# Performance work log

Measured on AMD Instinct MI355X. Metric: run time of the kernel, lower is better.

## Reference

```python
import jax, jax.numpy as jnp
import numpy as np

B, T, I = 32, 512, 1024
H, HS = 8, 128  # n_heads, head_size; hidden = H*HS = 1024
LIM = 1.0 / np.sqrt(HS)


def setup_inputs() -> dict:
    key = jax.random.key(0)
    kx, kif, kzo, khh, kb = jax.random.split(key, 5)
    u = lambda k, shp: jax.random.uniform(k, shp, jnp.float32, -LIM, LIM)
    return {
        "xs": jax.random.normal(kx, (B, T, I), jnp.float32),
        "weight_if": u(kif, (H, 2 * HS, I)),
        "weight_zo": u(kzo, (H, 2 * HS, I)),
        "weight_hh": u(khh, (H, 4 * HS, HS)),
        "bias": u(kb, (H, 4 * HS)),
    }


def reference(xs, weight_if, weight_zo, weight_hh, bias):
    # xs: [B, T, I]. Scan the sLSTM cell over time, batched over B via einsum.
    b, t, _ = xs.shape
    n_heads, four_hs, head_size = weight_hh.shape

    def step(state, x):  # x: [B, I]
        h, c, m, n = state  # each [B, H, HS]
        if_lin = jnp.einsum('hki,bi->bhk', weight_if, x)  # [B, H, 2*HS]
        zo_lin = jnp.einsum('hki,bi->bhk', weight_zo, x)  # [B, H, 2*HS]
        lin = jnp.concatenate([if_lin, zo_lin], axis=2)
        lin = lin + jnp.einsum('hkd,bhd->bhk', weight_hh, h) + bias  # [B, H, 4*HS]
        i, f, z, o = jnp.split(lin, 4, axis=2)
        z = jnp.tanh(z)
        o = jax.nn.sigmoid(o)
        m_new = jnp.maximum(f + m, i)          # stabilizer
        i_e = jnp.exp(i - m_new)
        f_e = jnp.exp(f + m - m_new)
        c_new = f_e * c + i_e * z
        n_new = f_e * n + i_e
        h_new = o * (c_new / n_new)
        return (h_new, c_new, m_new, n_new), h_new.reshape(b, n_heads * head_size)

    init = tuple(jnp.zeros((b, n_heads, head_size), xs.dtype) for _ in range(4))
    _, hs = jax.lax.scan(step, init, jnp.swapaxes(xs, 0, 1))  # hs: [T, B, hidden]
    return jnp.swapaxes(hs, 0, 1)  # [B, T, hidden]
```

## Files before the change

### kernel.cpp

```cpp
#include <hip/hip_runtime.h>
#include <hip/hip_bf16.h>
#include <stdint.h>

#define B_SZ 32
#define T_SZ 512
#define I_SZ 1024
#define H_SZ 8
#define HS_SZ 128

typedef __attribute__((ext_vector_type(8))) short short8;
typedef __attribute__((ext_vector_type(4))) float f32x4;
typedef __attribute__((ext_vector_type(2))) float f32x2;

static __device__ __forceinline__ unsigned short f2bf(float f) {
  union { float f; unsigned int u; } c; c.f = f;
  unsigned int u = c.u;
  unsigned int r = (u + 0x7fffu + ((u >> 16) & 1u)) >> 16;
  return (unsigned short)r;
}
static __device__ __forceinline__ float bf2f(unsigned short s) {
  union { unsigned int u; float f; } c; c.u = ((unsigned int)s) << 16;
  return c.f;
}
static __device__ __forceinline__ void split2(float x, unsigned short& hi,
                                              unsigned short& lo) {
  hi = f2bf(x);
  lo = f2bf(x - bf2f(hi));
}

__global__ void conv_x_split(const float* __restrict__ x,
                             unsigned short* __restrict__ ohi,
                             unsigned short* __restrict__ olo, int n4) {
  int i = blockIdx.x * blockDim.x + threadIdx.x;
  if (i >= n4) return;
  float4 v = ((const float4*)x)[i];
  ushort4 h, l;
  split2(v.x, h.x, l.x);
  split2(v.y, h.y, l.y);
  split2(v.z, h.z, l.z);
  split2(v.w, h.w, l.w);
  ((ushort4*)ohi)[i] = h;
  ((ushort4*)olo)[i] = l;
}

__global__ void conv_w_split(const float* __restrict__ wif,
                             const float* __restrict__ wzo,
                             unsigned short* __restrict__ ohi,
                             unsigned short* __restrict__ olo) {
  int i = blockIdx.x * blockDim.x + threadIdx.x;
  int flat = i * 4;
  int n = flat >> 10;
  int col = flat & 1023;
  int h = n >> 9, k4 = n & 511;
  const float* src = (k4 < 256)
                         ? (wif + ((size_t)(h * 256 + k4) * 1024 + col))
                         : (wzo + ((size_t)(h * 256 + (k4 - 256)) * 1024 + col));
  float4 v = *(const float4*)src;
  ushort4 hh, ll;
  split2(v.x, hh.x, ll.x);
  split2(v.y, hh.y, ll.y);
  split2(v.z, hh.z, ll.z);
  split2(v.w, hh.w, ll.w);
  ((ushort4*)ohi)[i] = hh;
  ((ushort4*)olo)[i] = ll;
}

__device__ __forceinline__ void gld_lds16(const void* g, void* l) {
  __builtin_amdgcn_global_load_lds(
      (const __attribute__((address_space(1))) void*)g,
      (__attribute__((address_space(3))) void*)l, 16, 0, 0);
}

__global__ __launch_bounds__(512)
void gemm3_kernel(const unsigned short* __restrict__ Ahi,
                  const unsigned short* __restrict__ Alo,
                  const unsigned short* __restrict__ Whi,
                  const unsigned short* __restrict__ Wlo,
                  float* __restrict__ G, int t0, int ltch) {
  __shared__ short lds2[2][24576];

  const int tid = threadIdx.x;
  const int lane = tid & 63, wv = tid >> 6;
  const int wm = wv >> 1, wn = wv & 1;
  const int bx = blockIdx.x, by = blockIdx.y;
  const int l15 = lane & 15, kg = lane >> 4;
  const int tchm = (1 << ltch) - 1;

  const unsigned short* gsrc[6];
#pragma unroll
  for (int t = 0; t < 6; ++t) {
    int u = tid + t * 512;
    int j = u & 3;
    if (t < 4) {
      int r = (u >> 2) & 255;
      int gslot = j ^ ((r >> 1) & 3);
      int cr = bx * 256 + r;
      size_t xsrow = (size_t)(cr >> ltch) * 512 + t0 + (cr & tchm);
      gsrc[t] = ((t < 2) ? Ahi : Alo) + xsrow * 1024 + gslot * 8;
    } else {
      int r = (u >> 2) & 127;
      int gslot = j ^ ((r >> 1) & 3);
      size_t wr = (size_t)by * 128 + r;
      gsrc[t] = ((t == 4) ? Whi : Wlo) + wr * 1024 + gslot * 8;
    }
  }

  int offa[4], offw[4];
#pragma unroll
  for (int mi = 0; mi < 4; ++mi) {
    int r = wm * 64 + mi * 16 + l15;
    offa[mi] = r * 32 + (kg ^ ((r >> 1) & 3)) * 8;
  }
#pragma unroll
  for (int ni = 0; ni < 4; ++ni) {
    int r = wn * 64 + ni * 16 + l15;
    offw[ni] = r * 32 + (kg ^ ((r >> 1) & 3)) * 8;
  }

  f32x4 zero4 = {0.f, 0.f, 0.f, 0.f};
  f32x4 acc[4][4];
#pragma unroll
  for (int mi = 0; mi < 4; ++mi)
#pragma unroll
    for (int ni = 0; ni < 4; ++ni) acc[mi][ni] = zero4;

#pragma unroll
  for (int t = 0; t < 6; ++t)
    gld_lds16(gsrc[t], &lds2[0][(wv * 64 + t * 512) * 8]);
#pragma unroll
  for (int t = 0; t < 6; ++t)
    gld_lds16(gsrc[t] + 32, &lds2[1][(wv * 64 + t * 512) * 8]);
  asm volatile("s_waitcnt vmcnt(6)" : : : "memory");
  __builtin_amdgcn_s_barrier();

  for (int ks = 0; ks < 32; ++ks) {
    const short* bp = &lds2[ks & 1][0];

    short8 ah[4], wh4[4], al[4], wl4[4];
#pragma unroll
    for (int mi = 0; mi < 4; ++mi) ah[mi] = *(const short8*)(bp + offa[mi]);
#pragma unroll
    for (int ni = 0; ni < 4; ++ni)
      wh4[ni] = *(const short8*)(bp + 16384 + offw[ni]);

    __builtin_amdgcn_s_setprio(1);
#pragma unroll
    for (int mi = 0; mi < 4; ++mi)
#pragma unroll
      for (int ni = 0; ni < 4; ++ni)
        acc[mi][ni] = __builtin_amdgcn_mfma_f32_16x16x32_bf16(
            ah[mi], wh4[ni], acc[mi][ni], 0, 0, 0);

#pragma unroll
    for (int mi = 0; mi < 4; ++mi)
      al[mi] = *(const short8*)(bp + 8192 + offa[mi]);
#pragma unroll
    for (int mi = 0; mi < 4; ++mi)
#pragma unroll
      for (int ni = 0; ni < 4; ++ni)
        acc[mi][ni] = __builtin_amdgcn_mfma_f32_16x16x32_bf16(
            al[mi], wh4[ni], acc[mi][ni], 0, 0, 0);

#pragma unroll
    for (int ni = 0; ni < 4; ++ni)
      wl4[ni] = *(const short8*)(bp + 20480 + offw[ni]);
#pragma unroll
    for (int mi = 0; mi < 4; ++mi)
#pragma unroll
      for (int ni = 0; ni < 4; ++ni)
        acc[mi][ni] = __builtin_amdgcn_mfma_f32_16x16x32_bf16(
            ah[mi], wl4[ni], acc[mi][ni], 0, 0, 0);
    __builtin_amdgcn_s_setprio(0);

    asm volatile("s_waitcnt lgkmcnt(0)" : : : "memory");
    __builtin_amdgcn_sched_barrier(0);
    __builtin_amdgcn_s_barrier();

    if (ks + 2 < 32) {
#pragma unroll
      for (int t = 0; t < 6; ++t)
        gld_lds16(gsrc[t] + (ks + 2) * 32,
                  &lds2[ks & 1][(wv * 64 + t * 512) * 8]);
      asm volatile("s_waitcnt vmcnt(6)" : : : "memory");
    } else {
      asm volatile("s_waitcnt vmcnt(0)" : : : "memory");
    }
    __builtin_amdgcn_s_barrier();
  }

#pragma unroll
  for (int mi = 0; mi < 4; ++mi)
#pragma unroll
    for (int ni = 0; ni < 4; ++ni)
#pragma unroll
      for (int r = 0; r < 4; ++r) {
        int grow = bx * 256 + wm * 64 + mi * 16 + kg * 4 + r;
        int gcol = by * 128 + wn * 64 + ni * 16 + l15;
        G[(size_t)grow * 4096 + gcol] = acc[mi][ni][r];
      }
}

__global__ __launch_bounds__(512, 1)
void recur_kernel(const float* __restrict__ G,
                  const float* __restrict__ Whh,
                  const float* __restrict__ bias,
                  float* __restrict__ out,
                  float* __restrict__ state,
                  int t0, int tch, int first) {
  int blk = blockIdx.x;
  int b = blk >> 3, h = blk & 7;
  int t = threadIdx.x;
  int w = t >> 6;
  int l = t & 63;
  int q = w >> 1;
  int em = (w & 1) * 64 + l;
  int eg = q * 32 + (l & 31);

  __shared__ __align__(16) float part[2][128 * 20];

  f32x2 w2[64];
  {
    const float* wb = Whh + (size_t)h * 65536 + (size_t)q * 32;
#pragma unroll
    for (int g = 0; g < 4; ++g) {
      const float4* wp = (const float4*)(wb + (size_t)(g * 128 + em) * 128);
#pragma unroll
      for (int c4 = 0; c4 < 8; ++c4) {
        float4 v = wp[c4];
        f32x2 lo2 = {v.x, v.y};
        f32x2 hi2 = {v.z, v.w};
        w2[g * 16 + 2 * c4] = lo2;
        w2[g * 16 + 2 * c4 + 1] = hi2;
      }
    }
  }
#pragma unroll
  for (int i = 0; i < 64; ++i)
    asm volatile("" : "+v"(w2[i]));

  int si = (b * 8 + h) * 128 + eg;
  float hreg = 0.f, c_r = 0.f, n_r = 0.f, m_r = 0.f;
  if (!first) {
    hreg = state[si];
    c_r = state[32768 + si];
    m_r = state[65536 + si];
    n_r = state[98304 + si];
  }
  float bj0 = bias[h * 512 + eg];
  float bj1 = bias[h * 512 + 128 + eg];
  float bj2 = bias[h * 512 + 256 + eg];
  float bj3 = bias[h * 512 + 384 + eg];

  const float* gpb = G + (size_t)(b * tch) * 4096 + h * 512 + eg;
  float* op = out + ((size_t)b * 512 + t0) * 1024 + h * 128 + eg;
  bool writer = ((w & 1) == 0) && (l < 32);

  int ebase = em * 20 + q * 4;
  int rb0 = eg * 20 + 0;
  int rb1 = eg * 20 + 4;
  int rb2 = eg * 20 + 8;
  int rb3 = eg * 20 + 12;

  float g0 = gpb[0], g1 = gpb[128], g2 = gpb[256], g3 = gpb[384];

  for (int s = 0; s < tch; ++s) {
    float gn0 = 0.f, gn1 = 0.f, gn2 = 0.f, gn3 = 0.f;
    if (s + 1 < tch) {
      const float* gr = gpb + (size_t)(s + 1) * 4096;
      gn0 = gr[0]; gn1 = gr[128]; gn2 = gr[256]; gn3 = gr[384];
    }

    f32x2 a0 = {0.f, 0.f}, a1 = {0.f, 0.f}, a2 = {0.f, 0.f}, a3 = {0.f, 0.f};
    int hbits = __float_as_int(hreg);
#pragma unroll
    for (int c2 = 0; c2 < 16; ++c2) {
      unsigned int hlo = (unsigned int)__builtin_amdgcn_readlane(hbits, 2 * c2);
      unsigned int hhi =
          (unsigned int)__builtin_amdgcn_readlane(hbits, 2 * c2 + 1);
      uint64_t h2 = ((uint64_t)hhi << 32) | (uint64_t)hlo;
      asm("v_pk_fma_f32 %0, %1, %2, %0" : "+v"(a0) : "v"(w2[c2]), "s"(h2));
      asm("v_pk_fma_f32 %0, %1, %2, %0" : "+v"(a1) : "v"(w2[16 + c2]), "s"(h2));
      asm("v_pk_fma_f32 %0, %1, %2, %0" : "+v"(a2) : "v"(w2[32 + c2]), "s"(h2));
      asm("v_pk_fma_f32 %0, %1, %2, %0" : "+v"(a3) : "v"(w2[48 + c2]), "s"(h2));
    }
    float4 pv = {a0.x + a0.y, a1.x + a1.y, a2.x + a2.y, a3.x + a3.y};
    *(float4*)&part[s & 1][ebase] = pv;
    __syncthreads();

    float4 p0 = *(const float4*)&part[s & 1][rb0];
    float4 p1 = *(const float4*)&part[s & 1][rb1];
    float4 p2 = *(const float4*)&part[s & 1][rb2];
    float4 p3 = *(const float4*)&part[s & 1][rb3];
    float iv = bj0 + g0 + ((p0.x + p1.x) + (p2.x + p3.x));
    float fv = bj1 + g1 + ((p0.y + p1.y) + (p2.y + p3.y));
    float zv = bj2 + g2 + ((p0.z + p1.z) + (p2.z + p3.z));
    float ov = bj3 + g3 + ((p0.w + p1.w) + (p2.w + p3.w));
    float e2 = __expf(2.f * zv);
    float zt = 1.f - 2.f * __builtin_amdgcn_rcpf(e2 + 1.f);
    float og = __builtin_amdgcn_rcpf(1.f + __expf(-ov));
    float mn = fmaxf(fv + m_r, iv);
    float ie = __expf(iv - mn);
    float fe = __expf(fv + m_r - mn);
    c_r = fe * c_r + ie * zt;
    n_r = fe * n_r + ie;
    m_r = mn;
    float hnew = og * c_r * __builtin_amdgcn_rcpf(n_r);
    hreg = hnew;
    if (writer) op[(size_t)s * 1024] = hnew;
    g0 = gn0; g1 = gn1; g2 = gn2; g3 = gn3;
  }

  if (writer) {
    state[si] = hreg;
    state[32768 + si] = c_r;
    state[65536 + si] = m_r;
    state[98304 + si] = n_r;
  }
}

extern "C" void kernel_launch(void* const* d_in, const int* in_sizes, int n_in,
                              void* d_out, int out_size, void* d_ws, size_t ws_size,
                              hipStream_t stream) {
  const float* xs   = (const float*)d_in[0];
  const float* wif  = (const float*)d_in[1];
  const float* wzo  = (const float*)d_in[2];
  const float* whh  = (const float*)d_in[3];
  const float* bias = (const float*)d_in[4];
  float* out = (float*)d_out;

  char* ws = (char*)d_ws;
  unsigned short* Ahi = (unsigned short*)ws;
  unsigned short* Alo = (unsigned short*)(ws + 33554432);
  unsigned short* Whi = (unsigned short*)(ws + 67108864);
  unsigned short* Wlo = (unsigned short*)(ws + 75497472);
  const size_t gbase = 83886080;

  int tch = 512;
  while (tch > 8 &&
         gbase + (size_t)32 * tch * 4096 * 4 + 524288 > ws_size)
    tch >>= 1;
  int ltch = 0;
  while ((1 << (ltch + 1)) <= tch) ++ltch;

  float* G = (float*)(ws + gbase);
  float* state = (float*)(ws + gbase + (size_t)32 * tch * 4096 * 4);

  conv_x_split<<<16384, 256, 0, stream>>>(xs, Ahi, Alo, 4194304);
  conv_w_split<<<4096, 256, 0, stream>>>(wif, wzo, Whi, Wlo);

  for (int t0 = 0; t0 < 512; t0 += tch) {
    gemm3_kernel<<<dim3((32 * tch) / 256, 32), 512, 0, stream>>>(
        Ahi, Alo, Whi, Wlo, G, t0, ltch);
    recur_kernel<<<256, 512, 0, stream>>>(G, whh, bias, out, state, t0, tch,
                                          t0 == 0);
  }
}
```

Baseline: 801.4 us.

## Batch 16 sequences per block and run recurrent matvec on bf16x3 MFMA

Replaces the per-(batch,head) scalar packed-FMA recurrence with a kernel where each block handles 16 batch rows of one head. The h·Whh product becomes an MFMA GEMM using a hi/lo bf16 split (three MFMA passes) with Whh held in registers and h exchanged through swizzled LDS. The partial-sum LDS reduction goes away and the launch shrinks from 256 to 16 blocks. The trade-offs are far less parallelism across CUs, a longer per-step critical path per block, and some loss of precision from the bf16 splitting.

```diff
diff --git a/kernel.cpp b/kernel.cpp
--- a/kernel.cpp
+++ b/kernel.cpp
@@ -10,7 +10,6 @@
 
 typedef __attribute__((ext_vector_type(8))) short short8;
 typedef __attribute__((ext_vector_type(4))) float f32x4;
-typedef __attribute__((ext_vector_type(2))) float f32x2;
 
 static __device__ __forceinline__ unsigned short f2bf(float f) {
   union { float f; unsigned int u; } c; c.f = f;
@@ -201,120 +200,180 @@
 }
 
 __global__ __launch_bounds__(512, 1)
-void recur_kernel(const float* __restrict__ G,
-                  const float* __restrict__ Whh,
-                  const float* __restrict__ bias,
-                  float* __restrict__ out,
-                  float* __restrict__ state,
-                  int t0, int tch, int first) {
-  int blk = blockIdx.x;
-  int b = blk >> 3, h = blk & 7;
-  int t = threadIdx.x;
-  int w = t >> 6;
-  int l = t & 63;
-  int q = w >> 1;
-  int em = (w & 1) * 64 + l;
-  int eg = q * 32 + (l & 31);
-
-  __shared__ __align__(16) float part[2][128 * 20];
-
-  f32x2 w2[64];
-  {
-    const float* wb = Whh + (size_t)h * 65536 + (size_t)q * 32;
-#pragma unroll
-    for (int g = 0; g < 4; ++g) {
-      const float4* wp = (const float4*)(wb + (size_t)(g * 128 + em) * 128);
-#pragma unroll
-      for (int c4 = 0; c4 < 8; ++c4) {
-        float4 v = wp[c4];
-        f32x2 lo2 = {v.x, v.y};
-        f32x2 hi2 = {v.z, v.w};
-        w2[g * 16 + 2 * c4] = lo2;
-        w2[g * 16 + 2 * c4 + 1] = hi2;
+void recur2_kernel(const float* __restrict__ G,
+                   const float* __restrict__ Whh,
+                   const float* __restrict__ bias,
+                   float* __restrict__ out,
+                   float* __restrict__ state,
+                   int t0, int tch, int first) {
+  const int blk = blockIdx.x;
+  const int g16 = (blk >> 3) * 16;
+  const int h = blk & 7;
+  const int t = threadIdx.x;
+  const int w = t >> 6, l = t & 63;
+  const int l15 = l & 15, kg = l >> 4;
+  const int e = w * 16 + l15;
+
+  __shared__ __align__(16) short hb[2][2][2048];
+
+  short8 wh[4][4], wl[4][4];
+#pragma unroll
+  for (int gt = 0; gt < 4; ++gt)
+#pragma unroll
+    for (int ks = 0; ks < 4; ++ks) {
+      const float* wp = Whh + (size_t)h * 65536 +
+                        (size_t)(gt * 128 + e) * 128 + ks * 32 + kg * 8;
+      float4 v0 = ((const float4*)wp)[0];
+      float4 v1 = ((const float4*)wp)[1];
+      float vv[8] = {v0.x, v0.y, v0.z, v0.w, v1.x, v1.y, v1.z, v1.w};
+      short8 hi8, lo8;
+#pragma unroll
+      for (int j = 0; j < 8; ++j) {
+        unsigned short hi, lo;
+        split2(vv[j], hi, lo);
+        hi8[j] = (short)hi;
+        lo8[j] = (short)lo;
       }
-    }
-  }
-#pragma unroll
-  for (int i = 0; i < 64; ++i)
-    asm volatile("" : "+v"(w2[i]));
-
-  int si = (b * 8 + h) * 128 + eg;
-  float hreg = 0.f, c_r = 0.f, n_r = 0.f, m_r = 0.f;
-  if (!first) {
-    hreg = state[si];
-    c_r = state[32768 + si];
-    m_r = state[65536 + si];
-    n_r = state[98304 + si];
-  }
-  float bj0 = bias[h * 512 + eg];
-  float bj1 = bias[h * 512 + 128 + eg];
-  float bj2 = bias[h * 512 + 256 + eg];
-  float bj3 = bias[h * 512 + 384 + eg];
-
-  const float* gpb = G + (size_t)(b * tch) * 4096 + h * 512 + eg;
-  float* op = out + ((size_t)b * 512 + t0) * 1024 + h * 128 + eg;
-  bool writer = ((w & 1) == 0) && (l < 32);
-
-  int ebase = em * 20 + q * 4;
-  int rb0 = eg * 20 + 0;
-  int rb1 = eg * 20 + 4;
-  int rb2 = eg * 20 + 8;
-  int rb3 = eg * 20 + 12;
-
-  float g0 = gpb[0], g1 = gpb[128], g2 = gpb[256], g3 = gpb[384];
+      wh[gt][ks] = hi8;
+      wl[gt][ks] = lo8;
+    }
+
+  float bj[4];
+#pragma unroll
+  for (int gt = 0; gt < 4; ++gt) bj[gt] = bias[h * 512 + gt * 128 + e];
+
+  size_t gbase_r[4], obase_r[4];
+  int sibase_r[4], woff[4];
+  const int u = e >> 3;
+#pragma unroll
+  for (int r = 0; r < 4; ++r) {
+    int b = kg * 4 + r;
+    gbase_r[r] = ((size_t)(g16 + b) * tch) * 4096 + h * 512 + e;
+    obase_r[r] = ((size_t)(g16 + b) * 512 + t0) * 1024 + h * 128 + e;
+    sibase_r[r] = ((g16 + b) * 8 + h) * 128 + e;
+    woff[r] = b * 128 +
+              (((((u >> 2) ^ kg) & 3) << 2) | (((u & 3) ^ r) & 3)) * 8 +
+              (e & 7);
+  }
+  int roA[4];
+#pragma unroll
+  for (int ks = 0; ks < 4; ++ks)
+    roA[ks] = l15 * 128 +
+              ((((ks ^ (l15 >> 2)) & 3) << 2) | ((kg ^ l15) & 3)) * 8;
+
+  float c_r[4] = {0.f, 0.f, 0.f, 0.f};
+  float n_r[4] = {0.f, 0.f, 0.f, 0.f};
+  float m_r[4] = {0.f, 0.f, 0.f, 0.f};
+  short* buf0 = &hb[0][0][0];
+#pragma unroll
+  for (int r = 0; r < 4; ++r) {
+    float h0 = 0.f;
+    if (!first) {
+      h0 = state[sibase_r[r]];
+      c_r[r] = state[32768 + sibase_r[r]];
+      m_r[r] = state[65536 + sibase_r[r]];
+      n_r[r] = state[98304 + sibase_r[r]];
+    }
+    unsigned short hhi, hlo;
+    split2(h0, hhi, hlo);
+    buf0[woff[r]] = (short)hhi;
+    buf0[2048 + woff[r]] = (short)hlo;
+  }
+
+  f32x4 gc[4];
+#pragma unroll
+  for (int gt = 0; gt < 4; ++gt)
+#pragma unroll
+    for (int r = 0; r < 4; ++r) gc[gt][r] = G[gbase_r[r] + gt * 128];
+
+  __syncthreads();
 
   for (int s = 0; s < tch; ++s) {
-    float gn0 = 0.f, gn1 = 0.f, gn2 = 0.f, gn3 = 0.f;
+    const short* bufr = &hb[s & 1][0][0];
+    short8 ahf[4], alf[4];
+#pragma unroll
+    for (int ks = 0; ks < 4; ++ks) {
+      ahf[ks] = *(const short8*)(bufr + roA[ks]);
+      alf[ks] = *(const short8*)(bufr + 2048 + roA[ks]);
+    }
+
+    f32x4 gn[4];
+#pragma unroll
+    for (int gt = 0; gt < 4; ++gt) {
+      f32x4 z = {0.f, 0.f, 0.f, 0.f};
+      gn[gt] = z;
+    }
     if (s + 1 < tch) {
-      const float* gr = gpb + (size_t)(s + 1) * 4096;
-      gn0 = gr[0]; gn1 = gr[128]; gn2 = gr[256]; gn3 = gr[384];
-    }
-
-    f32x2 a0 = {0.f, 0.f}, a1 = {0.f, 0.f}, a2 = {0.f, 0.f}, a3 = {0.f, 0.f};
-    int hbits = __float_as_int(hreg);
-#pragma unroll
-    for (int c2 = 0; c2 < 16; ++c2) {
-      unsigned int hlo = (unsigned int)__builtin_amdgcn_readlane(hbits, 2 * c2);
-      unsigned int hhi =
-          (unsigned int)__builtin_amdgcn_readlane(hbits, 2 * c2 + 1);
-      uint64_t h2 = ((uint64_t)hhi << 32) | (uint64_t)hlo;
-      asm("v_pk_fma_f32 %0, %1, %2, %0" : "+v"(a0) : "v"(w2[c2]), "s"(h2));
-      asm("v_pk_fma_f32 %0, %1, %2, %0" : "+v"(a1) : "v"(w2[16 + c2]), "s"(h2));
-      asm("v_pk_fma_f32 %0, %1, %2, %0" : "+v"(a2) : "v"(w2[32 + c2]), "s"(h2));
-      asm("v_pk_fma_f32 %0, %1, %2, %0" : "+v"(a3) : "v"(w2[48 + c2]), "s"(h2));
-    }
-    float4 pv = {a0.x + a0.y, a1.x + a1.y, a2.x + a2.y, a3.x + a3.y};
-    *(float4*)&part[s & 1][ebase] = pv;
+#pragma unroll
+      for (int gt = 0; gt < 4; ++gt)
+#pragma unroll
+        for (int r = 0; r < 4; ++r)
+          gn[gt][r] = G[gbase_r[r] + (size_t)(s + 1) * 4096 + gt * 128];
+    }
+
+    f32x4 acc[4];
+#pragma unroll
+    for (int gt = 0; gt < 4; ++gt)
+#pragma unroll
+      for (int r = 0; r < 4; ++r) acc[gt][r] = bj[gt] + gc[gt][r];
+
+    __builtin_amdgcn_s_setprio(1);
+#pragma unroll
+    for (int gt = 0; gt < 4; ++gt)
+#pragma unroll
+      for (int ks = 0; ks < 4; ++ks)
+        acc[gt] = __builtin_amdgcn_mfma_f32_16x16x32_bf16(
+            ahf[ks], wh[gt][ks], acc[gt], 0, 0, 0);
+#pragma unroll
+    for (int gt = 0; gt < 4; ++gt)
+#pragma unroll
+      for (int ks = 0; ks < 4; ++ks)
+        acc[gt] = __builtin_amdgcn_mfma_f32_16x16x32_bf16(
+            alf[ks], wh[gt][ks], acc[gt], 0, 0, 0);
+#pragma unroll
+    for (int gt = 0; gt < 4; ++gt)
+#pragma unroll
+      for (int ks = 0; ks < 4; ++ks)
+        acc[gt] = __builtin_amdgcn_mfma_f32_16x16x32_bf16(
+            ahf[ks], wl[gt][ks], acc[gt], 0, 0, 0);
+    __builtin_amdgcn_s_setprio(0);
+
+    short* bufw = &hb[(s + 1) & 1][0][0];
+#pragma unroll
+    for (int r = 0; r < 4; ++r) {
+      float iv = acc[0][r];
+      float fv = acc[1][r];
+      float zv = acc[2][r];
+      float ov = acc[3][r];
+      float e2 = __expf(2.f * zv);
+      float zt = 1.f - 2.f * __builtin_amdgcn_rcpf(e2 + 1.f);
+      float og = __builtin_amdgcn_rcpf(1.f + __expf(-ov));
+      float mn = fmaxf(fv + m_r[r], iv);
+      float ie = __expf(iv - mn);
+      float fe = __expf(fv + m_r[r] - mn);
+      c_r[r] = fe * c_r[r] + ie * zt;
+      n_r[r] = fe * n_r[r] + ie;
+      m_r[r] = mn;
+      float hnew = og * c_r[r] * __builtin_amdgcn_rcpf(n_r[r]);
+      out[obase_r[r] + (size_t)s * 1024] = hnew;
+      unsigned short hhi, hlo;
+      split2(hnew, hhi, hlo);
+      bufw[woff[r]] = (short)hhi;
+      bufw[2048 + woff[r]] = (short)hlo;
+    }
+#pragma unroll
+    for (int gt = 0; gt < 4; ++gt) gc[gt] = gn[gt];
     __syncthreads();
-
-    float4 p0 = *(const float4*)&part[s & 1][rb0];
-    float4 p1 = *(const float4*)&part[s & 1][rb1];
-    float4 p2 = *(const float4*)&part[s & 1][rb2];
-    float4 p3 = *(const float4*)&part[s & 1][rb3];
-    float iv = bj0 + g0 + ((p0.x + p1.x) + (p2.x + p3.x));
-    float fv = bj1 + g1 + ((p0.y + p1.y) + (p2.y + p3.y));
-    float zv = bj2 + g2 + ((p0.z + p1.z) + (p2.z + p3.z));
-    float ov = bj3 + g3 + ((p0.w + p1.w) + (p2.w + p3.w));
-    float e2 = __expf(2.f * zv);
-    float zt = 1.f - 2.f * __builtin_amdgcn_rcpf(e2 + 1.f);
-    float og = __builtin_amdgcn_rcpf(1.f + __expf(-ov));
-    float mn = fmaxf(fv + m_r, iv);
-    float ie = __expf(iv - mn);
-    float fe = __expf(fv + m_r - mn);
-    c_r = fe * c_r + ie * zt;
-    n_r = fe * n_r + ie;
-    m_r = mn;
-    float hnew = og * c_r * __builtin_amdgcn_rcpf(n_r);
-    hreg = hnew;
-    if (writer) op[(size_t)s * 1024] = hnew;
-    g0 = gn0; g1 = gn1; g2 = gn2; g3 = gn3;
-  }
-
-  if (writer) {
-    state[si] = hreg;
-    state[32768 + si] = c_r;
-    state[65536 + si] = m_r;
-    state[98304 + si] = n_r;
+  }
+
+#pragma unroll
+  for (int r = 0; r < 4; ++r) {
+    float hfin = bf2f((unsigned short)hb[tch & 1][0][woff[r]]) +
+                 bf2f((unsigned short)hb[tch & 1][1][woff[r]]);
+    state[sibase_r[r]] = hfin;
+    state[32768 + sibase_r[r]] = c_r[r];
+    state[65536 + sibase_r[r]] = m_r[r];
+    state[98304 + sibase_r[r]] = n_r[r];
   }
 }
 
@@ -351,7 +410,7 @@
   for (int t0 = 0; t0 < 512; t0 += tch) {
     gemm3_kernel<<<dim3((32 * tch) / 256, 32), 512, 0, stream>>>(
         Ahi, Alo, Whi, Wlo, G, t0, ltch);
-    recur_kernel<<<256, 512, 0, stream>>>(G, whh, bias, out, state, t0, tch,
+    recur2_kernel<<<16, 512, 0, stream>>>(G, whh, bias, out, state, t0, tch,
                                           t0 == 0);
   }
 }
```

After: 1.297 ms. 1.62x slower.
